# Optimization experiments

Hardware: AMD Instinct MI355X
Metric: run time of the kernel (lower is better)

Reference implementation:

```python
import jax, jax.numpy as jnp
import numpy as np

B, C, S = 32, 64, 112
RATIO = 8
EPS = 1e-5


def conv1x1(x, w, b):
    # 1x1 conv == channel-mixing matmul. x:[B,C,H,W], w:[O,C], b:[O]
    return jnp.einsum('oc,bchw->bohw', w, x) + b[None, :, None, None]


def dwconv(x, w, b):
    # grouped 1x1 conv with groups=C: per-channel scale + bias
    return x * w[None, :, None, None] + b[None, :, None, None]


def bn(x, g, b):
    # BatchNorm2d in training mode: batch stats over (N,H,W), biased var
    m = x.mean((0, 2, 3), keepdims=True)
    v = x.var((0, 2, 3), keepdims=True)
    return (x - m) * jax.lax.rsqrt(v + EPS) * g[None, :, None, None] + b[None, :, None, None]


def avgpool(x, k):
    # nn.AvgPool2d(k): kernel k, stride k, VALID (floor) padding
    s = jax.lax.reduce_window(x, 0.0, jax.lax.add, (1, 1, k, k), (1, 1, k, k), 'VALID')
    return s / float(k * k)


def setup_inputs() -> dict:
    key = jax.random.key(0)
    ks = jax.random.split(key, 20)
    C2, H = 2 * C, (2 * C) // RATIO

    def n(k, shape, s=0.02):
        return jax.random.normal(k, shape, jnp.float32) * s

    return {
        'rgb': jax.random.normal(ks[0], (B, C, S, S), jnp.float32),
        'fre': jax.random.normal(ks[1], (B, C, S, S), jnp.float32),
        'wq_fad': n(ks[2], (C, C)), 'bq_fad': jnp.zeros((C,), jnp.float32),
        'wq_lfs': n(ks[3], (C, C)), 'bq_lfs': jnp.zeros((C,), jnp.float32),
        'wk_fad': n(ks[4], (C, C)), 'bk_fad': jnp.zeros((C,), jnp.float32),
        'wk_lfs': n(ks[5], (C, C)), 'bk_lfs': jnp.zeros((C,), jnp.float32),
        'fad_gamma': n(ks[6], (1,), 1.0), 'lfs_gamma': n(ks[7], (1,), 1.0),
        'fad_cw': n(ks[8], (C,), 1.0), 'fad_cb': jnp.zeros((C,), jnp.float32),
        'fad_bg': jnp.ones((C,), jnp.float32), 'fad_bb': jnp.zeros((C,), jnp.float32),
        'lfs_cw': n(ks[9], (C,), 1.0), 'lfs_cb': jnp.zeros((C,), jnp.float32),
        'lfs_bg': jnp.ones((C,), jnp.float32), 'lfs_bb': jnp.zeros((C,), jnp.float32),
        'lin1_w': n(ks[10], (3,), 0.3), 'lin2_w': n(ks[11], (3,), 0.3),
        'mlp_w1': n(ks[12], (H, C2)), 'mlp_w2': n(ks[13], (C2, H)),
        'rgb_cw': n(ks[14], (C,), 1.0), 'rgb_cb': jnp.zeros((C,), jnp.float32),
        'rgb_bg': jnp.ones((C,), jnp.float32), 'rgb_bb': jnp.zeros((C,), jnp.float32),
        'fre_cw': n(ks[15], (C,), 1.0), 'fre_cb': jnp.zeros((C,), jnp.float32),
        'fre_bg': jnp.ones((C,), jnp.float32), 'fre_bb': jnp.zeros((C,), jnp.float32),
    }


def reference(rgb, fre, wq_fad, bq_fad, wq_lfs, bq_lfs, wk_fad, bk_fad, wk_lfs, bk_lfs,
              fad_gamma, lfs_gamma, fad_cw, fad_cb, fad_bg, fad_bb,
              lfs_cw, lfs_cb, lfs_bg, lfs_bb, lin1_w, lin2_w, mlp_w1, mlp_w2,
              rgb_cw, rgb_cb, rgb_bg, rgb_bb, fre_cw, fre_cb, fre_bg, fre_bb):
    Bn, Cn, Sz, _ = rgb.shape
    # ---- MixBlock: cross attention over folded (B*C) batch ----
    qF = conv1x1(rgb, wq_fad, bq_fad).reshape(Bn * Cn, Sz, Sz)
    qL = conv1x1(fre, wq_lfs, bq_lfs).reshape(Bn * Cn, Sz, Sz)
    Mq = jnp.concatenate([qF, qL], axis=2)          # [BC, S, 2S]
    kF = conv1x1(rgb, wk_fad, bk_fad).reshape(Bn * Cn, Sz, Sz).transpose(0, 2, 1)
    kL = conv1x1(fre, wk_lfs, bk_lfs).reshape(Bn * Cn, Sz, Sz).transpose(0, 2, 1)
    Mk = jnp.concatenate([kF, kL], axis=1)          # [BC, 2S, S]
    attn = jax.nn.softmax(jnp.matmul(Mq, Mk), axis=-1).reshape(Bn, Cn, Sz, Sz)
    att_lfs = fre * attn * (jax.nn.sigmoid(lfs_gamma) * 2.0 - 1.0)
    y_fad = rgb + bn(dwconv(att_lfs, fad_cw, fad_cb), fad_bg, fad_bb)
    att_fad = rgb * attn * (jax.nn.sigmoid(fad_gamma) * 2.0 - 1.0)
    y_lfs = fre + bn(dwconv(att_fad, lfs_cw, lfs_cb), lfs_bg, lfs_bb)
    # ---- MSCA on concatenated channels ----
    x = jnp.concatenate([y_fad, y_lfs], axis=1)     # [B, 2C, S, S]
    avgs, maxs = [], []
    for k in (3, 5, 7):
        m = avgpool(x, k)
        avgs.append(m.mean((2, 3)))
        maxs.append(m.max((2, 3)))
    a_p = jnp.stack(avgs, -1) @ lin1_w              # [B, 2C]
    m_p = jnp.stack(maxs, -1) @ lin2_w

    def mlp(v):
        h = jax.nn.relu(jnp.einsum('rc,bc->br', mlp_w1, v))
        return jnp.einsum('cr,br->bc', mlp_w2, h)

    ca = jax.nn.sigmoid(mlp(a_p) + mlp(m_p))        # [B, 2C]
    r_c = ca[:, :Cn, None, None]
    f_c = ca[:, Cn:, None, None]
    rgb_out = y_fad + bn(dwconv(r_c * y_fad, rgb_cw, rgb_cb), rgb_bg, rgb_bb)
    fre_out = y_lfs + bn(dwconv(f_c * y_lfs, fre_cw, fre_cb), fre_bg, fre_bb)
    return (rgb_out, fre_out)
```

## Files before the change

kernel.cpp:

```cpp
#include <hip/hip_runtime.h>
#include <hip/hip_bf16.h>
#include <stdint.h>

#define NE 25690112ull
#define PP 12544
#define SS 112
#define EPSV 1e-5f

typedef __attribute__((ext_vector_type(8))) short short8v;
typedef __attribute__((ext_vector_type(4))) float float4v;

__device__ __forceinline__ unsigned short f2bf(float x){
  union { float f; uint32_t u; } v; v.f = x;
  uint32_t r = (v.u + 0x7fffu + ((v.u >> 16) & 1u)) >> 16;
  return (unsigned short)r;
}
__device__ __forceinline__ float bf2f(unsigned short u){ return __uint_as_float(((uint32_t)u) << 16); }

__global__ __launch_bounds__(256) void k1_conv(
    const float* __restrict__ rgb, const float* __restrict__ fre,
    const float* __restrict__ wq_fad, const float* __restrict__ bq_fad,
    const float* __restrict__ wk_fad, const float* __restrict__ bk_fad,
    const float* __restrict__ wq_lfs, const float* __restrict__ bq_lfs,
    const float* __restrict__ wk_lfs, const float* __restrict__ bk_lfs,
    unsigned short* __restrict__ qF, unsigned short* __restrict__ kF,
    unsigned short* __restrict__ qL, unsigned short* __restrict__ kL,
    unsigned short* __restrict__ rgbb, unsigned short* __restrict__ freb)
{
  const int bx = blockIdx.x, b = blockIdx.y, z = blockIdx.z;
  const float* X  = z ? fre : rgb;
  const float* Wq = z ? wq_lfs : wq_fad;
  const float* Bq = z ? bq_lfs : bq_fad;
  const float* Wk = z ? wk_lfs : wk_fad;
  const float* Bk = z ? bk_lfs : bk_fad;
  unsigned short* Oq = z ? qL : qF;
  unsigned short* Ok = z ? kL : kF;
  unsigned short* Xb = z ? freb : rgbb;

  __shared__ __align__(16) unsigned short xs[64 * 260];

  const int tid = threadIdx.x, lane = tid & 63, w = tid >> 6;
  const int lc = lane & 15, l4 = lane >> 4;

  const int p0 = bx*256;
  const size_t xbase = (size_t)b * 64 * PP;
  #pragma unroll
  for (int i = 0; i < 16; ++i){
    const int c = w*16 + i;
    const size_t gof = xbase + (size_t)c*PP + p0 + lane*4;
    float4 xv = *(const float4*)(X + gof);
    ushort4 s;
    s.x = f2bf(xv.x); s.y = f2bf(xv.y); s.z = f2bf(xv.z); s.w = f2bf(xv.w);
    *(ushort4*)(Xb + gof) = s;
    *(ushort4*)(&xs[c*260 + lane*4]) = s;
  }
  __syncthreads();

  short8v afr[4][2];
  #pragma unroll
  for (int t = 0; t < 4; ++t){
    const int p = (t*4 + w)*16 + lc;
    #pragma unroll
    for (int ks = 0; ks < 2; ++ks){
      short8v a;
      #pragma unroll
      for (int j = 0; j < 8; ++j)
        a[j] = (short)xs[(ks*32 + l4*8 + j)*260 + p];
      afr[t][ks] = a;
    }
  }
  __syncthreads();

  #pragma unroll
  for (int arr = 0; arr < 2; ++arr){
    const float* W = arr ? Wk : Wq;
    const float* Bi = arr ? Bk : Bq;
    unsigned short* O = arr ? Ok : Oq;
    short8v wf[4][2];
    float bias[4];
    #pragma unroll
    for (int ot = 0; ot < 4; ++ot){
      bias[ot] = Bi[ot*16 + lc];
      #pragma unroll
      for (int ks = 0; ks < 2; ++ks){
        const int base = (ot*16 + lc)*64 + ks*32 + l4*8;
        const float4 q0 = *(const float4*)(W + base);
        const float4 q1 = *(const float4*)(W + base + 4);
        short8v v;
        v[0]=(short)f2bf(q0.x); v[1]=(short)f2bf(q0.y); v[2]=(short)f2bf(q0.z); v[3]=(short)f2bf(q0.w);
        v[4]=(short)f2bf(q1.x); v[5]=(short)f2bf(q1.y); v[6]=(short)f2bf(q1.z); v[7]=(short)f2bf(q1.w);
        wf[ot][ks] = v;
      }
    }
    #pragma unroll
    for (int t = 0; t < 4; ++t){
      const int pt = (t*4 + w)*16;
      #pragma unroll
      for (int ot = 0; ot < 4; ++ot){
        float4v acc = (float4v){bias[ot], bias[ot], bias[ot], bias[ot]};
        acc = __builtin_amdgcn_mfma_f32_16x16x32_bf16(afr[t][0], wf[ot][0], acc, 0, 0, 0);
        acc = __builtin_amdgcn_mfma_f32_16x16x32_bf16(afr[t][1], wf[ot][1], acc, 0, 0, 0);
        ushort4 u;
        u.x = f2bf(acc[0]); u.y = f2bf(acc[1]); u.z = f2bf(acc[2]); u.w = f2bf(acc[3]);
        const int o = ot*16 + lc;
        uint32_t byteS = (uint32_t)(o*512 + (pt + l4*4)*2) ^ (uint32_t)((o & 7) << 4);
        *(ushort4*)((char*)xs + byteS) = u;
      }
    }
    __syncthreads();
    for (int i = tid; i < 2048; i += 256){
      const int o = i >> 5, s = i & 31;
      uint32_t byteS = (uint32_t)(o*512 + s*16) ^ (uint32_t)((o & 7) << 4);
      short8v v = *(const short8v*)((const char*)xs + byteS);
      *(short8v*)(O + ((size_t)b*64 + o)*PP + p0 + s*8) = v;
    }
    __syncthreads();
  }
}

__global__ __launch_bounds__(448) void k2_attn(
    unsigned short* __restrict__ qF, const unsigned short* __restrict__ qL,
    const unsigned short* __restrict__ kF, const unsigned short* __restrict__ kL,
    const unsigned short* __restrict__ rgbb, const unsigned short* __restrict__ freb,
    const float* __restrict__ fad_gamma, const float* __restrict__ lfs_gamma,
    float* __restrict__ stats)
{
  const int bc = blockIdx.x, c = bc & 63;
  const size_t plane = (size_t)bc * PP;
  __shared__ __align__(16) unsigned short ksF[112][128];
  __shared__ __align__(16) unsigned short ksL[112][128];
  const int tid = threadIdx.x, lane = tid & 63, w = tid >> 6;
  const int l4 = lane >> 4, lc = lane & 15;

  const uint32_t* kFu = (const uint32_t*)kF + plane/2;
  const uint32_t* kLu = (const uint32_t*)kL + plane/2;
  for (int i = tid; i < 7168; i += 448){
    int row = i >> 6, wd = i & 63;
    uint32_t vF = (wd < 56) ? kFu[row*56 + wd] : 0u;
    uint32_t vL = (wd < 56) ? kLu[row*56 + wd] : 0u;
    uint32_t byteS = (uint32_t)((row << 8) | (wd << 2)) ^ (uint32_t)((row & 7) << 4);
    *(uint32_t*)((char*)&ksF[0][0] + byteS) = vF;
    *(uint32_t*)((char*)&ksL[0][0] + byteS) = vL;
  }
  __syncthreads();

  float4v acc[7];
  #pragma unroll
  for (int ct = 0; ct < 7; ++ct) acc[ct] = (float4v)0.f;

  const unsigned short* qFp = qF + plane;
  const unsigned short* qLp = qL + plane;
  const int qrow = w*16 + lc;
  #pragma unroll
  for (int ks = 0; ks < 4; ++ks){
    short8v aF = (short8v)(short)0, aL = (short8v)(short)0;
    const int joff = ks*32 + l4*8;
    if ((ks < 3) || (l4 < 2)){
      aF = *(const short8v*)(qFp + qrow*SS + joff);
      aL = *(const short8v*)(qLp + qrow*SS + joff);
    }
    #pragma unroll
    for (int ct = 0; ct < 7; ++ct){
      uint32_t byteS = (uint32_t)((ct*16 + lc)*256 + ks*64 + l4*16) ^ (uint32_t)((lc & 7) << 4);
      short8v bF = *(const short8v*)((const char*)&ksF[0][0] + byteS);
      short8v bL = *(const short8v*)((const char*)&ksL[0][0] + byteS);
      acc[ct] = __builtin_amdgcn_mfma_f32_16x16x32_bf16(aF, bF, acc[ct], 0, 0, 0);
      acc[ct] = __builtin_amdgcn_mfma_f32_16x16x32_bf16(aL, bL, acc[ct], 0, 0, 0);
    }
  }

  const float sF = 2.f/(1.f + __expf(-fad_gamma[0])) - 1.f;
  const float sL = 2.f/(1.f + __expf(-lfs_gamma[0])) - 1.f;
  unsigned short* attnP = qF + plane;
  unsigned short* alin = &ksF[0][0];

  __syncthreads();
  #pragma unroll
  for (int r = 0; r < 4; ++r){
    const int i = w*16 + l4*4 + r;
    float v[7];
    #pragma unroll
    for (int ct = 0; ct < 7; ++ct) v[ct] = acc[ct][r];
    float m = fmaxf(fmaxf(fmaxf(v[0],v[1]),fmaxf(v[2],v[3])), fmaxf(fmaxf(v[4],v[5]),v[6]));
    #pragma unroll
    for (int off = 8; off; off >>= 1) m = fmaxf(m, __shfl_xor(m, off, 64));
    float e[7]; float s = 0.f;
    #pragma unroll
    for (int ct = 0; ct < 7; ++ct){ e[ct] = __expf(v[ct] - m); s += e[ct]; }
    #pragma unroll
    for (int off = 8; off; off >>= 1) s += __shfl_xor(s, off, 64);
    const float inv = 1.f / s;
    #pragma unroll
    for (int ct = 0; ct < 7; ++ct)
      alin[i*SS + ct*16 + lc] = f2bf(e[ct] * inv);
  }
  __syncthreads();

  float ls1 = 0.f, lq1 = 0.f, ls2 = 0.f, lq2 = 0.f;
  for (int i4 = tid; i4 < 3136; i4 += 448){
    ushort4 av = *(const ushort4*)(alin + i4*4);
    *(ushort4*)(attnP + (size_t)i4*4) = av;
    ushort4 fr = *(const ushort4*)(freb + plane + (size_t)i4*4);
    ushort4 rg = *(const ushort4*)(rgbb + plane + (size_t)i4*4);
    const unsigned short* ap = &av.x;
    const unsigned short* fp = &fr.x;
    const unsigned short* rp = &rg.x;
    #pragma unroll
    for (int j = 0; j < 4; ++j){
      float a = bf2f(ap[j]);
      float v1 = bf2f(fp[j]) * a * sL;
      float v2 = bf2f(rp[j]) * a * sF;
      ls1 += v1; lq1 += v1*v1; ls2 += v2; lq2 += v2*v2;
    }
  }
  #pragma unroll
  for (int off = 32; off; off >>= 1){
    ls1 += __shfl_xor(ls1, off, 64);
    lq1 += __shfl_xor(lq1, off, 64);
    ls2 += __shfl_xor(ls2, off, 64);
    lq2 += __shfl_xor(lq2, off, 64);
  }
  if (lane == 0){
    atomicAdd(&stats[c],       ls1);
    atomicAdd(&stats[64 + c],  lq1);
    atomicAdd(&stats[128 + c], ls2);
    atomicAdd(&stats[192 + c], lq2);
  }
}

__global__ void k3_affine1(const float* __restrict__ stats,
    const float* __restrict__ fad_cw, const float* __restrict__ fad_bg, const float* __restrict__ fad_bb,
    const float* __restrict__ lfs_cw, const float* __restrict__ lfs_bg, const float* __restrict__ lfs_bb,
    float* __restrict__ AB)
{
  int c = threadIdx.x;
  if (c >= 64) return;
  const float n = 401408.f;
  {
    float m1 = stats[c]/n, v1 = stats[64+c]/n - (stats[c]/n)*(stats[c]/n);
    float cw = fad_cw[c], g = fad_bg[c];
    float rs = rsqrtf(cw*cw*v1 + EPSV);
    AB[c]      = cw*rs*g;
    AB[64 + c] = -cw*m1*rs*g + fad_bb[c];
  }
  {
    float m2 = stats[128+c]/n, v2 = stats[192+c]/n - (stats[128+c]/n)*(stats[128+c]/n);
    float cw = lfs_cw[c], g = lfs_bg[c];
    float rs = rsqrtf(cw*cw*v2 + EPSV);
    AB[128 + c] = cw*rs*g;
    AB[192 + c] = -cw*m2*rs*g + lfs_bb[c];
  }
}

__global__ __launch_bounds__(512) void k4_fuse(
    const unsigned short* __restrict__ attn,
    const unsigned short* __restrict__ rgbb, const unsigned short* __restrict__ freb,
    const float* __restrict__ AB1,
    const float* __restrict__ fad_gamma, const float* __restrict__ lfs_gamma,
    unsigned short* __restrict__ ybf, unsigned short* __restrict__ ybl,
    float* __restrict__ avgstat, float* __restrict__ maxstat,
    float4* __restrict__ planeStats)
{
  const int bc = blockIdx.x, b = bc >> 6, c = bc & 63;
  const size_t plane = (size_t)bc * PP;
  __shared__ unsigned short ys[2][112][113];
  __shared__ float redA[8][4];
  __shared__ float redS[8], redM[8];
  const int tid = threadIdx.x, lane = tid & 63, w = tid >> 6;
  const float sF = 2.f/(1.f + __expf(-fad_gamma[0])) - 1.f;
  const float sL = 2.f/(1.f + __expf(-lfs_gamma[0])) - 1.f;
  const float A1 = AB1[c], B1 = AB1[64+c], A2 = AB1[128+c], B2 = AB1[192+c];
  float s0 = 0.f, q0 = 0.f, s1 = 0.f, q1 = 0.f;

  for (int i4 = tid; i4 < 3136; i4 += 512){
    ushort4 av = *(const ushort4*)(attn + plane + (size_t)i4*4);
    ushort4 rg = *(const ushort4*)(rgbb + plane + (size_t)i4*4);
    ushort4 fr = *(const ushort4*)(freb + plane + (size_t)i4*4);
    float aa[4] = {bf2f(av.x), bf2f(av.y), bf2f(av.z), bf2f(av.w)};
    float rr[4] = {bf2f(rg.x), bf2f(rg.y), bf2f(rg.z), bf2f(rg.w)};
    float ff[4] = {bf2f(fr.x), bf2f(fr.y), bf2f(fr.z), bf2f(fr.w)};
    float y0[4], y1[4];
    ushort4 o0, o1;
    unsigned short* p0 = &o0.x; unsigned short* p1 = &o1.x;
    #pragma unroll
    for (int j = 0; j < 4; ++j){
      float t1 = ff[j]*aa[j]*sL;
      float t2 = rr[j]*aa[j]*sF;
      y0[j] = rr[j] + A1*t1 + B1;
      y1[j] = ff[j] + A2*t2 + B2;
      s0 += y0[j]; q0 += y0[j]*y0[j];
      s1 += y1[j]; q1 += y1[j]*y1[j];
      p0[j] = f2bf(y0[j]);
      p1[j] = f2bf(y1[j]);
    }
    *(ushort4*)(ybf + plane + (size_t)i4*4) = o0;
    *(ushort4*)(ybl + plane + (size_t)i4*4) = o1;
    int r = i4 / 28, c0 = (i4 % 28) * 4;
    #pragma unroll
    for (int j = 0; j < 4; ++j){
      ys[0][r][c0+j] = p0[j];
      ys[1][r][c0+j] = p1[j];
    }
  }
  #pragma unroll
  for (int off = 32; off; off >>= 1){
    s0 += __shfl_xor(s0, off, 64); q0 += __shfl_xor(q0, off, 64);
    s1 += __shfl_xor(s1, off, 64); q1 += __shfl_xor(q1, off, 64);
  }
  if (lane == 0){ redA[w][0] = s0; redA[w][1] = q0; redA[w][2] = s1; redA[w][3] = q1; }
  __syncthreads();
  if (tid == 0){
    float a0=0,a1=0,a2=0,a3=0;
    for (int i = 0; i < 8; ++i){ a0+=redA[i][0]; a1+=redA[i][1]; a2+=redA[i][2]; a3+=redA[i][3]; }
    float4 ps = {a0,a1,a2,a3};
    planeStats[bc] = ps;
  }
  __syncthreads();

  const int kk[3] = {3,5,7};
  const int gg[3] = {37,22,16};
  for (int pl = 0; pl < 2; ++pl){
    const int cc = pl*64 + c;
    for (int ki = 0; ki < 3; ++ki){
      const int k = kk[ki], g = gg[ki];
      float sumAll = 0.f, mx = -3.0e38f;
      for (int win = tid; win < g*g; win += 512){
        int wy = win / g, wx = win % g;
        float s = 0.f;
        for (int dy = 0; dy < k; ++dy)
          for (int dx = 0; dx < k; ++dx)
            s += bf2f(ys[pl][wy*k+dy][wx*k+dx]);
        sumAll += s; mx = fmaxf(mx, s);
      }
      #pragma unroll
      for (int off = 32; off; off >>= 1){
        sumAll += __shfl_xor(sumAll, off, 64);
        mx = fmaxf(mx, __shfl_xor(mx, off, 64));
      }
      if (lane == 0){ redS[w] = sumAll; redM[w] = mx; }
      __syncthreads();
      if (tid == 0){
        float st = 0.f, mt = -3.0e38f;
        for (int i = 0; i < 8; ++i){ st += redS[i]; mt = fmaxf(mt, redM[i]); }
        int idx = (b*128 + cc)*3 + ki;
        avgstat[idx] = st / (float)(k*k*g*g);
        maxstat[idx] = mt / (float)(k*k);
      }
      __syncthreads();
    }
  }
}

__global__ void k6_mlp(const float* __restrict__ avgstat, const float* __restrict__ maxstat,
    const float* __restrict__ lin1, const float* __restrict__ lin2,
    const float* __restrict__ w1, const float* __restrict__ w2,
    float* __restrict__ ca)
{
  const int b = blockIdx.x, tid = threadIdx.x;
  __shared__ float sa[128], sm[128], hA[16], hM[16];
  int idx = (b*128 + tid)*3;
  sa[tid] = avgstat[idx]*lin1[0] + avgstat[idx+1]*lin1[1] + avgstat[idx+2]*lin1[2];
  sm[tid] = maxstat[idx]*lin2[0] + maxstat[idx+1]*lin2[1] + maxstat[idx+2]*lin2[2];
  __syncthreads();
  if (tid < 16){
    float ha = 0.f, hm = 0.f;
    for (int c2 = 0; c2 < 128; ++c2){
      ha += w1[tid*128 + c2]*sa[c2];
      hm += w1[tid*128 + c2]*sm[c2];
    }
    hA[tid] = fmaxf(ha, 0.f); hM[tid] = fmaxf(hm, 0.f);
  }
  __syncthreads();
  float o = 0.f;
  for (int r = 0; r < 16; ++r) o += w2[tid*16 + r]*(hA[r] + hM[r]);
  ca[b*128 + tid] = 1.f/(1.f + __expf(-o));
}

__global__ void k8_affineF(const float4* __restrict__ planeStats, const float* __restrict__ ca,
    const float* __restrict__ rgb_cw, const float* __restrict__ rgb_bg, const float* __restrict__ rgb_bb,
    const float* __restrict__ fre_cw, const float* __restrict__ fre_bg, const float* __restrict__ fre_bb,
    float* __restrict__ ABF)
{
  int t = threadIdx.x;
  if (t >= 128) return;
  int z = t >> 6, c = t & 63;
  float S = 0.f, Q = 0.f;
  for (int b = 0; b < 32; ++b){
    float4 ps = planeStats[b*64 + c];
    float sc = ca[b*128 + t];
    float sp = z ? ps.z : ps.x;
    float qp = z ? ps.w : ps.y;
    S += sc*sp; Q += sc*sc*qp;
  }
  const float n = 401408.f;
  float m = S/n, v = Q/n - m*m;
  float cw = z ? fre_cw[c] : rgb_cw[c];
  float g  = z ? fre_bg[c] : rgb_bg[c];
  float bb = z ? fre_bb[c] : rgb_bb[c];
  float rs = rsqrtf(cw*cw*v + EPSV);
  ABF[z*128 + c]      = cw*rs*g;
  ABF[z*128 + 64 + c] = -cw*m*rs*g + bb;
}

__global__ __launch_bounds__(256) void k9_out(
    const unsigned short* __restrict__ ybf, const unsigned short* __restrict__ ybl,
    const float* __restrict__ ca, const float* __restrict__ ABF,
    float* __restrict__ out)
{
  const int c = blockIdx.x, b = blockIdx.y, z = blockIdx.z;
  const size_t plane = ((size_t)b*64 + c)*PP;
  const unsigned short* y = z ? ybl : ybf;
  float* o = out + (z ? NE : 0) + plane;
  const float sc = ca[b*128 + z*64 + c];
  const float A = ABF[z*128 + c], Bv = ABF[z*128 + 64 + c];
  const float mul = 1.f + A*sc;
  for (int i8 = threadIdx.x; i8 < 1568; i8 += 256){
    short8v yv = *(const short8v*)(y + plane + (size_t)i8*8);
    float4 o0, o1;
    o0.x = bf2f((unsigned short)yv[0])*mul + Bv;
    o0.y = bf2f((unsigned short)yv[1])*mul + Bv;
    o0.z = bf2f((unsigned short)yv[2])*mul + Bv;
    o0.w = bf2f((unsigned short)yv[3])*mul + Bv;
    o1.x = bf2f((unsigned short)yv[4])*mul + Bv;
    o1.y = bf2f((unsigned short)yv[5])*mul + Bv;
    o1.z = bf2f((unsigned short)yv[6])*mul + Bv;
    o1.w = bf2f((unsigned short)yv[7])*mul + Bv;
    *(float4*)(&o[(size_t)i8*8])     = o0;
    *(float4*)(&o[(size_t)i8*8 + 4]) = o1;
  }
}

extern "C" void kernel_launch(void* const* d_in, const int* in_sizes, int n_in,
                              void* d_out, int out_size, void* d_ws, size_t ws_size,
                              hipStream_t stream)
{
  (void)in_sizes; (void)n_in; (void)out_size; (void)ws_size;
  const float* rgb      = (const float*)d_in[0];
  const float* fre      = (const float*)d_in[1];
  const float* wq_fad   = (const float*)d_in[2];
  const float* bq_fad   = (const float*)d_in[3];
  const float* wq_lfs   = (const float*)d_in[4];
  const float* bq_lfs   = (const float*)d_in[5];
  const float* wk_fad   = (const float*)d_in[6];
  const float* bk_fad   = (const float*)d_in[7];
  const float* wk_lfs   = (const float*)d_in[8];
  const float* bk_lfs   = (const float*)d_in[9];
  const float* fad_gamma= (const float*)d_in[10];
  const float* lfs_gamma= (const float*)d_in[11];
  const float* fad_cw   = (const float*)d_in[12];
  const float* fad_bg   = (const float*)d_in[14];
  const float* fad_bb   = (const float*)d_in[15];
  const float* lfs_cw   = (const float*)d_in[16];
  const float* lfs_bg   = (const float*)d_in[18];
  const float* lfs_bb   = (const float*)d_in[19];
  const float* lin1_w   = (const float*)d_in[20];
  const float* lin2_w   = (const float*)d_in[21];
  const float* mlp_w1   = (const float*)d_in[22];
  const float* mlp_w2   = (const float*)d_in[23];
  const float* rgb_cw   = (const float*)d_in[24];
  const float* rgb_bg   = (const float*)d_in[26];
  const float* rgb_bb   = (const float*)d_in[27];
  const float* fre_cw   = (const float*)d_in[28];
  const float* fre_bg   = (const float*)d_in[30];
  const float* fre_bb   = (const float*)d_in[31];

  char* ws = (char*)d_ws;
  unsigned short* qF = (unsigned short*)(ws);
  unsigned short* qL = (unsigned short*)(ws + 2*NE);
  unsigned short* kF = (unsigned short*)(ws + 4*NE);
  unsigned short* kL = (unsigned short*)(ws + 6*NE);
  float* sbase = (float*)(ws + 8*NE);
  float* stats      = sbase;
  float* AB1        = sbase + 256;
  float* avgstat    = sbase + 512;
  float* maxstat    = sbase + 12800;
  float* ca         = sbase + 25088;
  float* ABF        = sbase + 29184;
  float4* planeStats= (float4*)(sbase + 29440);
  unsigned short* rgbb = (unsigned short*)d_out;
  unsigned short* freb = (unsigned short*)d_out + NE;

  hipMemsetAsync(stats, 0, 256*sizeof(float), stream);

  k1_conv<<<dim3(49,32,2), dim3(256), 0, stream>>>(rgb, fre,
      wq_fad, bq_fad, wk_fad, bk_fad, wq_lfs, bq_lfs, wk_lfs, bk_lfs,
      qF, kF, qL, kL, rgbb, freb);
  k2_attn<<<dim3(2048), dim3(448), 0, stream>>>(qF, qL, kF, kL,
      rgbb, freb, fad_gamma, lfs_gamma, stats);
  k3_affine1<<<dim3(1), dim3(64), 0, stream>>>(stats,
      fad_cw, fad_bg, fad_bb, lfs_cw, lfs_bg, lfs_bb, AB1);
  k4_fuse<<<dim3(2048), dim3(512), 0, stream>>>((const unsigned short*)qF,
      rgbb, freb, AB1, fad_gamma, lfs_gamma, kF, kL, avgstat, maxstat, planeStats);
  k6_mlp<<<dim3(32), dim3(128), 0, stream>>>(avgstat, maxstat,
      lin1_w, lin2_w, mlp_w1, mlp_w2, ca);
  k8_affineF<<<dim3(1), dim3(128), 0, stream>>>(planeStats, ca,
      rgb_cw, rgb_bg, rgb_bb, fre_cw, fre_bg, fre_bb, ABF);
  k9_out<<<dim3(64,32,2), dim3(256), 0, stream>>>(kF, kL, ca, ABF,
      (float*)d_out);
}
```

Before: 425.0 us.

## Prefetch Q fragments and rgb/fre tiles early, unpadded linear K staging in LDS

The attention kernel now loads the Q fragments into registers before staging K, and stages K into LDS as a flat unpadded copy (row stride 224 bytes, no XOR swizzle) with a fully unrolled loop. It also prefetches the rgb/fre bf16 tiles for the epilogue into registers during the MFMA phase, so that global latency overlaps with compute and softmax. The cost is higher register pressure, which could lower occupancy for the 448-thread blocks. The unswizzled 224-byte stride may also cause LDS bank conflicts on the B-fragment reads, and the last tile reads past row 111 into the 16-element padding.

```diff
diff --git a/kernel.cpp b/kernel.cpp
--- a/kernel.cpp
+++ b/kernel.cpp
@@ -127,52 +127,66 @@
 {
   const int bc = blockIdx.x, c = bc & 63;
   const size_t plane = (size_t)bc * PP;
-  __shared__ __align__(16) unsigned short ksF[112][128];
-  __shared__ __align__(16) unsigned short ksL[112][128];
+  __shared__ __align__(16) unsigned short ksF[PP + 16];
+  __shared__ __align__(16) unsigned short ksL[PP + 16];
   const int tid = threadIdx.x, lane = tid & 63, w = tid >> 6;
   const int l4 = lane >> 4, lc = lane & 15;
-
-  const uint32_t* kFu = (const uint32_t*)kF + plane/2;
-  const uint32_t* kLu = (const uint32_t*)kL + plane/2;
-  for (int i = tid; i < 7168; i += 448){
-    int row = i >> 6, wd = i & 63;
-    uint32_t vF = (wd < 56) ? kFu[row*56 + wd] : 0u;
-    uint32_t vL = (wd < 56) ? kLu[row*56 + wd] : 0u;
-    uint32_t byteS = (uint32_t)((row << 8) | (wd << 2)) ^ (uint32_t)((row & 7) << 4);
-    *(uint32_t*)((char*)&ksF[0][0] + byteS) = vF;
-    *(uint32_t*)((char*)&ksL[0][0] + byteS) = vL;
-  }
-  __syncthreads();
-
-  float4v acc[7];
-  #pragma unroll
-  for (int ct = 0; ct < 7; ++ct) acc[ct] = (float4v)0.f;
 
   const unsigned short* qFp = qF + plane;
   const unsigned short* qLp = qL + plane;
   const int qrow = w*16 + lc;
+  short8v aF[4], aL[4];
   #pragma unroll
   for (int ks = 0; ks < 4; ++ks){
-    short8v aF = (short8v)(short)0, aL = (short8v)(short)0;
     const int joff = ks*32 + l4*8;
     if ((ks < 3) || (l4 < 2)){
-      aF = *(const short8v*)(qFp + qrow*SS + joff);
-      aL = *(const short8v*)(qLp + qrow*SS + joff);
-    }
+      aF[ks] = *(const short8v*)(qFp + qrow*SS + joff);
+      aL[ks] = *(const short8v*)(qLp + qrow*SS + joff);
+    } else {
+      aF[ks] = (short8v)(short)0;
+      aL[ks] = (short8v)(short)0;
+    }
+  }
+
+  const uint32_t* kFu = (const uint32_t*)kF + plane/2;
+  const uint32_t* kLu = (const uint32_t*)kL + plane/2;
+  uint32_t* ksFw = (uint32_t*)ksF;
+  uint32_t* ksLw = (uint32_t*)ksL;
+  #pragma unroll
+  for (int t = 0; t < 14; ++t){
+    const int i = tid + t*448;
+    ksFw[i] = kFu[i];
+    ksLw[i] = kLu[i];
+  }
+  __syncthreads();
+
+  float4v acc[7];
+  #pragma unroll
+  for (int ct = 0; ct < 7; ++ct) acc[ct] = (float4v)0.f;
+  #pragma unroll
+  for (int ks = 0; ks < 4; ++ks){
     #pragma unroll
     for (int ct = 0; ct < 7; ++ct){
-      uint32_t byteS = (uint32_t)((ct*16 + lc)*256 + ks*64 + l4*16) ^ (uint32_t)((lc & 7) << 4);
-      short8v bF = *(const short8v*)((const char*)&ksF[0][0] + byteS);
-      short8v bL = *(const short8v*)((const char*)&ksL[0][0] + byteS);
-      acc[ct] = __builtin_amdgcn_mfma_f32_16x16x32_bf16(aF, bF, acc[ct], 0, 0, 0);
-      acc[ct] = __builtin_amdgcn_mfma_f32_16x16x32_bf16(aL, bL, acc[ct], 0, 0, 0);
-    }
+      const uint32_t off = (uint32_t)((ct*16 + lc)*224 + ks*64 + l4*16);
+      short8v bF = *(const short8v*)((const char*)ksF + off);
+      short8v bL = *(const short8v*)((const char*)ksL + off);
+      acc[ct] = __builtin_amdgcn_mfma_f32_16x16x32_bf16(aF[ks], bF, acc[ct], 0, 0, 0);
+      acc[ct] = __builtin_amdgcn_mfma_f32_16x16x32_bf16(aL[ks], bL, acc[ct], 0, 0, 0);
+    }
+  }
+
+  ushort4 frv[7], rgv[7];
+  #pragma unroll
+  for (int t = 0; t < 7; ++t){
+    const int i4 = tid + t*448;
+    frv[t] = *(const ushort4*)(freb + plane + (size_t)i4*4);
+    rgv[t] = *(const ushort4*)(rgbb + plane + (size_t)i4*4);
   }
 
   const float sF = 2.f/(1.f + __expf(-fad_gamma[0])) - 1.f;
   const float sL = 2.f/(1.f + __expf(-lfs_gamma[0])) - 1.f;
   unsigned short* attnP = qF + plane;
-  unsigned short* alin = &ksF[0][0];
+  unsigned short* alin = ksF;
 
   __syncthreads();
   #pragma unroll
@@ -197,14 +211,14 @@
   __syncthreads();
 
   float ls1 = 0.f, lq1 = 0.f, ls2 = 0.f, lq2 = 0.f;
-  for (int i4 = tid; i4 < 3136; i4 += 448){
+  #pragma unroll
+  for (int t = 0; t < 7; ++t){
+    const int i4 = tid + t*448;
     ushort4 av = *(const ushort4*)(alin + i4*4);
     *(ushort4*)(attnP + (size_t)i4*4) = av;
-    ushort4 fr = *(const ushort4*)(freb + plane + (size_t)i4*4);
-    ushort4 rg = *(const ushort4*)(rgbb + plane + (size_t)i4*4);
     const unsigned short* ap = &av.x;
-    const unsigned short* fp = &fr.x;
-    const unsigned short* rp = &rg.x;
+    const unsigned short* fp = &frv[t].x;
+    const unsigned short* rp = &rgv[t].x;
     #pragma unroll
     for (int j = 0; j < 4; ++j){
       float a = bf2f(ap[j]);
```

Result: faster. 399.4 us (-6.0%).
